# Kernel tuning notes

Measured on AMD Instinct MI355X. Metric: run time of the kernel, lower is better.

Reference implementation:

```python
import jax, jax.numpy as jnp
import numpy as np

N = 1024      # node_num
E = 4         # edge_type_num
D = 64        # state_dim
ANN = 16      # annotation_dim
STEPS = 5     # n_steps
B = 4         # batch


def setup_inputs() -> dict:
    key = jax.random.key(0)
    ks = jax.random.split(key, 10)
    w = lambda k, shape: jax.random.normal(k, shape, jnp.float32) * 0.02
    return {
        "prop_state": jax.random.normal(ks[0], (B, N, D), jnp.float32),
        "annotation": jax.random.normal(ks[1], (B, N, ANN), jnp.float32),
        "A": jax.random.uniform(ks[2], (B, N, 2 * N * E), jnp.float32),
        # per-edge-type linears (torch Linear: weight [out, in])
        "in_W": w(ks[3], (E, D, D)), "in_b": jnp.zeros((E, D), jnp.float32),
        "out_W": w(ks[4], (E, D, D)), "out_b": jnp.zeros((E, D), jnp.float32),
        # GRU-style gates: Linear(3D -> D)
        "rW": w(ks[5], (D, 3 * D)), "rb": jnp.zeros((D,), jnp.float32),
        "zW": w(ks[6], (D, 3 * D)), "zb": jnp.zeros((D,), jnp.float32),
        "hW": w(ks[7], (D, 3 * D)), "hb": jnp.zeros((D,), jnp.float32),
        # output head: Linear(D+ANN -> D) -> tanh -> Linear(D -> 1)
        "o1W": w(ks[8], (D, D + ANN)), "o1b": jnp.zeros((D,), jnp.float32),
        "o2W": w(ks[9], (1, D)), "o2b": jnp.zeros((1,), jnp.float32),
    }


def reference(prop_state, annotation, A, in_W, in_b, out_W, out_b,
              rW, rb, zW, zb, hW, hb, o1W, o1b, o2W, o2b):
    A_in = A[:, :, : N * E]  # [B, N, E*N]; A_out slice is unused in the original
    h = prop_state
    for _ in range(STEPS):
        # all edge-type linears as one batched GEMM: [B, N, E, D] -> [B, E*N, D]
        in_states = jnp.einsum("bnd,efd->bend", h, in_W) + in_b[None, :, None, :]
        in_states = in_states.reshape(B, E * N, D)
        a_in = jnp.einsum("bnm,bmd->bnd", A_in, in_states)
        a_out = a_in  # faithful to original: a_out = bmm(A_in, state_in) too
        a = jnp.concatenate([a_in, a_out, h], axis=2)  # [B, N, 3D]
        r = jax.nn.sigmoid(a @ rW.T + rb)
        z = jax.nn.sigmoid(a @ zW.T + zb)
        h_hat = jnp.tanh(jnp.concatenate([a_in, a_out, r * h], axis=2) @ hW.T + hb)
        h = (1.0 - z) * h + z * h_hat
    join = jnp.concatenate([h, annotation], axis=2)  # [B, N, D+ANN]
    out = jnp.tanh(join @ o1W.T + o1b) @ o2W.T + o2b  # [B, N, 1]
    return out.sum(axis=2)  # [B, N]
```

## Files before the change

### kernel.cpp

```cpp
#include <hip/hip_runtime.h>
#include <math.h>

#define N_NODES 1024
#define EDGE    4
#define DIM     64
#define ANND    16
#define STEPS   5
#define BATCH   4

typedef __attribute__((ext_vector_type(8))) short bf16x8;
typedef __attribute__((ext_vector_type(4))) float f32x4;

__device__ __forceinline__ float fsigmoid(float x) {
    return 1.0f / (1.0f + __expf(-x));
}
__device__ __forceinline__ float ftanh(float x) {
    x = fminf(15.0f, fmaxf(-15.0f, x));
    float t = __expf(2.0f * x);
    return (t - 1.0f) / (t + 1.0f);
}
__device__ __forceinline__ unsigned short f32_to_bf16(float x) {
    unsigned int u = __float_as_uint(x);
    unsigned int r = u + 0x7FFFu + ((u >> 16) & 1u);
    return (unsigned short)(r >> 16);
}

__global__ __launch_bounds__(256) void prepA(
    const float* __restrict__ A, unsigned short* __restrict__ Ahl,
    float* __restrict__ rowsum)
{
    const int row = blockIdx.x;
    const int t = threadIdx.x;
    const float* src = A + (size_t)row * 8192 + t * 16;
    unsigned short* dst = Ahl + (size_t)row * 8192 + t * 32;
    float s = 0.f;
#pragma unroll
    for (int c = 0; c < 2; ++c) {
        alignas(16) unsigned short hs[8], ls[8];
#pragma unroll
        for (int i = 0; i < 2; ++i) {
            float4 v = *(const float4*)(src + c * 8 + i * 4);
            float vv[4] = {v.x, v.y, v.z, v.w};
#pragma unroll
            for (int j = 0; j < 4; ++j) {
                float x = vv[j];
                s += x;
                unsigned short hh = f32_to_bf16(x);
                hs[i * 4 + j] = hh;
                ls[i * 4 + j] = f32_to_bf16(x - __uint_as_float((unsigned int)hh << 16));
            }
        }
        *(uint4*)(dst + c * 16)     = *(const uint4*)hs;
        *(uint4*)(dst + c * 16 + 8) = *(const uint4*)ls;
    }
#pragma unroll
    for (int off = 32; off > 0; off >>= 1) s += __shfl_down(s, off);
    if ((t & 63) == 0) rowsum[(size_t)row * 4 + (t >> 6)] = s;
}

__global__ void prepW(const float* __restrict__ inW, const float* __restrict__ rW,
                      const float* __restrict__ zW, const float* __restrict__ hW,
                      const float* __restrict__ o1W,
                      float* __restrict__ wcomb, float* __restrict__ w1s,
                      float* __restrict__ o1hT, float* __restrict__ o1aT)
{
    int id = blockIdx.x * 256 + threadIdx.x;
    if (id < 256) {
        int e = id >> 6, d = id & 63;
        float s = 0.0f;
        for (int f = 0; f < 64; ++f) s += inW[(e * 64 + f) * 64 + d];
        w1s[id] = s;
    }
    int i1 = id - 256;
    if (i1 >= 0 && i1 < 24576) {
        int mat = i1 >> 12, rem = i1 & 4095, d = rem >> 6, j = rem & 63;
        const float* W = (mat < 2) ? rW : (mat < 4) ? zW : hW;
        float v;
        if ((mat & 1) == 0) v = W[j * 192 + d] + W[j * 192 + 64 + d];
        else                v = W[j * 192 + 128 + d];
        wcomb[mat * 4096 + d * 64 + j] = v;
    }
    int i2 = id - 256 - 24576;
    if (i2 >= 0 && i2 < 4096) {
        int d = i2 >> 6, j = i2 & 63;
        o1hT[d * 64 + j] = o1W[j * 80 + d];
    }
    int i3 = id - 256 - 24576 - 4096;
    if (i3 >= 0 && i3 < 1024) {
        int a = i3 >> 6, j = i3 & 63;
        o1aT[a * 64 + j] = o1W[j * 80 + 64 + a];
    }
}

__global__ __launch_bounds__(256) void transposeH(
    const float* __restrict__ h, unsigned short* __restrict__ hThi,
    unsigned short* __restrict__ hTlo)
{
    __shared__ float tile[64][65];
    const int bm = blockIdx.x & 15, b = blockIdx.x >> 4;
    const int t = threadIdx.x;
    {
        const int mml = t >> 2, d0 = (t & 3) * 16;
        const float* src = h + ((size_t)(b * 1024 + bm * 64 + mml)) * 64 + d0;
#pragma unroll
        for (int i = 0; i < 4; ++i) {
            float4 v = *(const float4*)(src + i * 4);
            tile[d0 + i * 4 + 0][mml] = v.x;
            tile[d0 + i * 4 + 1][mml] = v.y;
            tile[d0 + i * 4 + 2][mml] = v.z;
            tile[d0 + i * 4 + 3][mml] = v.w;
        }
    }
    __syncthreads();
    const int d = t >> 2, m0 = (t & 3) * 16;
    alignas(16) unsigned short hb[16], lb[16];
#pragma unroll
    for (int i = 0; i < 16; ++i) {
        float x = tile[d][m0 + i];
        unsigned short hh = f32_to_bf16(x);
        hb[i] = hh;
        lb[i] = f32_to_bf16(x - __uint_as_float((unsigned int)hh << 16));
    }
    unsigned short* dst = hThi + ((size_t)(b * 64 + d)) * 1024 + bm * 64 + m0;
    *(uint4*)dst = *(const uint4*)&hb[0];
    *(uint4*)(dst + 8) = *(const uint4*)&hb[8];
    unsigned short* dstl = hTlo + ((size_t)(b * 64 + d)) * 1024 + bm * 64 + m0;
    *(uint4*)dstl = *(const uint4*)&lb[0];
    *(uint4*)(dstl + 8) = *(const uint4*)&lb[8];
}

__global__ __launch_bounds__(256, 4) void gemm_mfma(
    const unsigned short* __restrict__ Ahl,
    const unsigned short* __restrict__ hThi, const unsigned short* __restrict__ hTlo,
    const float* __restrict__ w1s, float* __restrict__ part)
{
    __shared__ unsigned short Xhs[64][64];
    __shared__ unsigned short Xls[64][64];
    const int tid = threadIdx.x;
    const int lane = tid & 63, wave = tid >> 6;
    const int nb = blockIdx.x, chunk = blockIdx.y, b = blockIdx.z;
    const int e = chunk >> 2, kq = chunk & 3;
    const int rowbase = nb * 64 + wave * 16;

    const size_t abase = ((size_t)(b * 1024 + rowbase + (lane & 15))) * 8192
                       + (size_t)(e * 128 + kq * 32 + (lane >> 4)) * 16;

    const int sd = tid >> 3;
    const int sc = tid & 7;
    const int scp = (sc ^ (sd & 7)) * 8;
    const int ldsoff0 = sd * 64 + scp;
    const int ldsoff1 = (sd + 32) * 64 + scp;
    const size_t xsrc = ((size_t)(b * 64 + sd)) * 1024 + kq * 256 + sc * 8;
    const unsigned short* xh0 = hThi + xsrc;
    const unsigned short* xl0 = hTlo + xsrc;

    uint4 sH0 = *(const uint4*)(xh0);
    uint4 sH1 = *(const uint4*)(xh0 + 32 * 1024);
    uint4 sL0 = *(const uint4*)(xl0);
    uint4 sL1 = *(const uint4*)(xl0 + 32 * 1024);

    f32x4 acc[4] = {};

#pragma unroll
    for (int sub = 0; sub < 4; ++sub) {
        __syncthreads();
        *(uint4*)&((unsigned short*)Xhs)[ldsoff0] = sH0;
        *(uint4*)&((unsigned short*)Xhs)[ldsoff1] = sH1;
        *(uint4*)&((unsigned short*)Xls)[ldsoff0] = sL0;
        *(uint4*)&((unsigned short*)Xls)[ldsoff1] = sL1;
        __syncthreads();
        if (sub < 3) {
            const unsigned short* ph = xh0 + (sub + 1) * 64;
            const unsigned short* pl = xl0 + (sub + 1) * 64;
            sH0 = *(const uint4*)(ph);
            sH1 = *(const uint4*)(ph + 32 * 1024);
            sL0 = *(const uint4*)(pl);
            sL1 = *(const uint4*)(pl + 32 * 1024);
        }
#pragma unroll
        for (int ks = 0; ks < 2; ++ks) {
            const unsigned short* ap = Ahl + abase + (size_t)(sub * 8 + ks * 4) * 16;
            bf16x8 a_hi = *(const bf16x8*)(ap);
            bf16x8 a_lo = *(const bf16x8*)(ap + 8);
#pragma unroll
            for (int df = 0; df < 4; ++df) {
                const int d = df * 16 + (lane & 15);
                const int cp = (((ks * 4) + (lane >> 4)) ^ (d & 7)) * 8;
                bf16x8 xh = *(const bf16x8*)&Xhs[d][cp];
                bf16x8 xl = *(const bf16x8*)&Xls[d][cp];
                acc[df] = __builtin_amdgcn_mfma_f32_16x16x32_bf16(a_hi, xh, acc[df], 0, 0, 0);
                acc[df] = __builtin_amdgcn_mfma_f32_16x16x32_bf16(a_hi, xl, acc[df], 0, 0, 0);
                acc[df] = __builtin_amdgcn_mfma_f32_16x16x32_bf16(a_lo, xh, acc[df], 0, 0, 0);
            }
        }
    }

    float* pbase = part + ((size_t)(chunk * 4 + b)) * 65536;
#pragma unroll
    for (int df = 0; df < 4; ++df) {
        const int d = df * 16 + (lane & 15);
        const float w = w1s[e * 64 + d];
#pragma unroll
        for (int r = 0; r < 4; ++r) {
            int n = rowbase + (lane >> 4) * 4 + r;
            pbase[(size_t)n * 64 + d] = acc[df][r] * w;
        }
    }
}

__global__ __launch_bounds__(256) void gate(
    const float* __restrict__ part, const float* __restrict__ wcomb,
    const float* __restrict__ rowsum, const float* __restrict__ inb,
    const float* __restrict__ rb, const float* __restrict__ zb,
    const float* __restrict__ hbias, float* __restrict__ h,
    unsigned short* __restrict__ hThi, unsigned short* __restrict__ hTlo)
{
    __shared__ float wl[24576];
    __shared__ float ain_sh[16][64];
    __shared__ float h_sh[16][64];
    __shared__ float r_sh[16][64];
    __shared__ float hn_sh[16][64];
    const int tid = threadIdx.x;
    const int nodeBase = blockIdx.x * 16;

#pragma unroll
    for (int i = 0; i < 24; ++i) {
        int idx = i * 256 + tid;
        *(float4*)&wl[idx * 4] = *(const float4*)&wcomb[idx * 4];
    }

#pragma unroll
    for (int i = 0; i < 4; ++i) {
        int idx = tid + 256 * i;
        int nl = idx >> 6, d = idx & 63;
        int node = nodeBase + nl;
        int bb = node >> 10, n = node & 1023;
        const float* pp = part + (size_t)bb * 65536 + (size_t)n * 64 + d;
        float s = 0.f;
#pragma unroll
        for (int c = 0; c < 16; ++c) s += pp[(size_t)c * 262144];
        const float* rs = rowsum + (size_t)node * 4;
#pragma unroll
        for (int e = 0; e < 4; ++e) s += rs[e] * inb[e * 64 + d];
        ain_sh[nl][d] = s;
        h_sh[nl][d] = h[(size_t)node * 64 + d];
    }
    __syncthreads();

    const int j  = tid & 63;
    const int ng = tid >> 6;
    const float* rCT = wl;
    const float* rHT = wl + 4096;
    const float* zCT = wl + 8192;
    const float* zHT = wl + 12288;
    const float* hCT = wl + 16384;
    const float* hHT = wl + 20480;

    float accr[4], accz[4];
#pragma unroll
    for (int i = 0; i < 4; ++i) { accr[i] = rb[j]; accz[i] = zb[j]; }
    for (int d = 0; d < 64; ++d) {
        float wrc = rCT[d * 64 + j], wrh = rHT[d * 64 + j];
        float wzc = zCT[d * 64 + j], wzh = zHT[d * 64 + j];
#pragma unroll
        for (int i = 0; i < 4; ++i) {
            int nl = ng * 4 + i;
            float av = ain_sh[nl][d], hv = h_sh[nl][d];
            accr[i] = fmaf(av, wrc, accr[i]); accr[i] = fmaf(hv, wrh, accr[i]);
            accz[i] = fmaf(av, wzc, accz[i]); accz[i] = fmaf(hv, wzh, accz[i]);
        }
    }
    float zreg[4];
#pragma unroll
    for (int i = 0; i < 4; ++i) {
        int nl = ng * 4 + i;
        r_sh[nl][j] = fsigmoid(accr[i]);
        zreg[i] = fsigmoid(accz[i]);
    }
    __syncthreads();

    float acch[4];
#pragma unroll
    for (int i = 0; i < 4; ++i) acch[i] = hbias[j];
    for (int d = 0; d < 64; ++d) {
        float whc = hCT[d * 64 + j], whh = hHT[d * 64 + j];
#pragma unroll
        for (int i = 0; i < 4; ++i) {
            int nl = ng * 4 + i;
            float av = ain_sh[nl][d];
            float rh = r_sh[nl][d] * h_sh[nl][d];
            acch[i] = fmaf(av, whc, acch[i]); acch[i] = fmaf(rh, whh, acch[i]);
        }
    }
#pragma unroll
    for (int i = 0; i < 4; ++i) {
        int nl = ng * 4 + i;
        int node = nodeBase + nl;
        float hh = ftanh(acch[i]);
        float ho = h_sh[nl][j];
        float hnew = ho + zreg[i] * (hh - ho);
        h[(size_t)node * 64 + j] = hnew;
        hn_sh[nl][j] = hnew;
    }
    __syncthreads();

    {
        const int d = tid >> 2, q = tid & 3;
        const int bb = nodeBase >> 10;
        const int mm0 = (nodeBase & 1023) + q * 4;
        alignas(8) unsigned short hb4[4], lb4[4];
#pragma unroll
        for (int i = 0; i < 4; ++i) {
            float x = hn_sh[q * 4 + i][d];
            unsigned short hh = f32_to_bf16(x);
            hb4[i] = hh;
            lb4[i] = f32_to_bf16(x - __uint_as_float((unsigned int)hh << 16));
        }
        unsigned short* dst = hThi + ((size_t)(bb * 64 + d)) * 1024 + mm0;
        *(uint2*)dst = *(const uint2*)hb4;
        unsigned short* dstl = hTlo + ((size_t)(bb * 64 + d)) * 1024 + mm0;
        *(uint2*)dstl = *(const uint2*)lb4;
    }
}

__global__ __launch_bounds__(256) void outk(
    const float* __restrict__ h, const float* __restrict__ ann,
    const float* __restrict__ o1hT, const float* __restrict__ o1aT,
    const float* __restrict__ o1b, const float* __restrict__ o2W,
    const float* __restrict__ o2b, float* __restrict__ out)
{
    __shared__ float h_sh[4][64];
    __shared__ float a_sh[4][16];
    const int tid = threadIdx.x;
    const int nodeBase = blockIdx.x * 4;
    {
        int nl = tid >> 6, d = tid & 63;
        h_sh[nl][d] = h[(size_t)(nodeBase + nl) * 64 + d];
    }
    if (tid < 64) {
        int nl = tid >> 4, a = tid & 15;
        a_sh[nl][a] = ann[(size_t)(nodeBase + nl) * 16 + a];
    }
    __syncthreads();
    const int j = tid & 63, nl = tid >> 6;
    float acc = o1b[j];
    for (int d = 0; d < 64; ++d) acc = fmaf(h_sh[nl][d], o1hT[d * 64 + j], acc);
    for (int a = 0; a < 16; ++a) acc = fmaf(a_sh[nl][a], o1aT[a * 64 + j], acc);
    float t = ftanh(acc) * o2W[j];
    for (int off = 32; off > 0; off >>= 1) t += __shfl_down(t, off);
    if (j == 0) out[nodeBase + nl] = t + o2b[0];
}

extern "C" void kernel_launch(void* const* d_in, const int* in_sizes, int n_in,
                              void* d_out, int out_size, void* d_ws, size_t ws_size,
                              hipStream_t stream)
{
    (void)in_sizes; (void)n_in; (void)out_size; (void)ws_size;
    const float* prop = (const float*)d_in[0];
    const float* ann  = (const float*)d_in[1];
    const float* A    = (const float*)d_in[2];
    const float* inW  = (const float*)d_in[3];
    const float* inb  = (const float*)d_in[4];
    const float* rW   = (const float*)d_in[7];
    const float* rb   = (const float*)d_in[8];
    const float* zW   = (const float*)d_in[9];
    const float* zb   = (const float*)d_in[10];
    const float* hW   = (const float*)d_in[11];
    const float* hb   = (const float*)d_in[12];
    const float* o1W  = (const float*)d_in[13];
    const float* o1b  = (const float*)d_in[14];
    const float* o2W  = (const float*)d_in[15];
    const float* o2b  = (const float*)d_in[16];
    float* out = (float*)d_out;

    float* h_ws   = (float*)d_ws;
    float* part   = h_ws + 262144;
    float* wcomb  = part + 16 * 262144;
    float* w1s    = wcomb + 24576;
    float* o1hT   = w1s + 256;
    float* o1aT   = o1hT + 4096;
    float* rowsum = o1aT + 1024;
    unsigned short* Ahl  = (unsigned short*)(rowsum + 16384);
    unsigned short* hThi = Ahl + (size_t)33554432;
    unsigned short* hTlo = hThi + 262144;

    prepA<<<4096, 256, 0, stream>>>(A, Ahl, rowsum);
    prepW<<<117, 256, 0, stream>>>(inW, rW, zW, hW, o1W, wcomb, w1s, o1hT, o1aT);
    hipMemcpyAsync(h_ws, prop, (size_t)262144 * sizeof(float),
                   hipMemcpyDeviceToDevice, stream);
    transposeH<<<64, 256, 0, stream>>>(h_ws, hThi, hTlo);

    for (int s = 0; s < STEPS; ++s) {
        gemm_mfma<<<dim3(16, 16, 4), 256, 0, stream>>>(Ahl, hThi, hTlo, w1s, part);
        gate<<<256, 256, 0, stream>>>(part, wcomb, rowsum, inb, rb, zb, hb,
                                      h_ws, hThi, hTlo);
    }
    outk<<<1024, 256, 0, stream>>>(h_ws, ann, o1hT, o1aT, o1b, o2W, o2b, out);
}
```

Baseline: 403.9 us.

## Fuse all stages into one persistent cooperative kernel with grid syncs

Replaces the chain of prep, per-step GEMM, gate and output kernels with a single cooperative kernel of 256 blocks that synchronises across the grid between phases. Each GEMM block now covers a full edge-type K range (16 sub-tiles) rather than a quarter, which shrinks the partial-sum buffer and the gate reduction. The gate weights are loaded into LDS once and reused across all steps. This removes about a dozen launches and their gaps, but runs only 256 blocks of heavy-LDS work, so GEMM parallelism drops and the A conversion pass loops over 16 rows per block.

```diff
diff --git a/kernel.cpp b/kernel.cpp
--- a/kernel.cpp
+++ b/kernel.cpp
@@ -1,5 +1,8 @@
 #include <hip/hip_runtime.h>
+#include <hip/hip_cooperative_groups.h>
 #include <math.h>
+
+namespace cg = cooperative_groups;
 
 #define N_NODES 1024
 #define EDGE    4
@@ -25,330 +28,344 @@
     return (unsigned short)(r >> 16);
 }
 
-__global__ __launch_bounds__(256) void prepA(
-    const float* __restrict__ A, unsigned short* __restrict__ Ahl,
-    float* __restrict__ rowsum)
+__global__ __launch_bounds__(256) void ggnn_mono(
+    const float* __restrict__ prop, const float* __restrict__ ann,
+    const float* __restrict__ A,
+    const float* __restrict__ inW, const float* __restrict__ inb,
+    const float* __restrict__ rW, const float* __restrict__ rb,
+    const float* __restrict__ zW, const float* __restrict__ zb,
+    const float* __restrict__ hW, const float* __restrict__ hb,
+    const float* __restrict__ o1W, const float* __restrict__ o1b,
+    const float* __restrict__ o2W, const float* __restrict__ o2b,
+    float* __restrict__ out, char* __restrict__ ws)
 {
-    const int row = blockIdx.x;
-    const int t = threadIdx.x;
-    const float* src = A + (size_t)row * 8192 + t * 16;
-    unsigned short* dst = Ahl + (size_t)row * 8192 + t * 32;
-    float s = 0.f;
-#pragma unroll
-    for (int c = 0; c < 2; ++c) {
-        alignas(16) unsigned short hs[8], ls[8];
-#pragma unroll
-        for (int i = 0; i < 2; ++i) {
-            float4 v = *(const float4*)(src + c * 8 + i * 4);
-            float vv[4] = {v.x, v.y, v.z, v.w};
-#pragma unroll
-            for (int j = 0; j < 4; ++j) {
-                float x = vv[j];
-                s += x;
-                unsigned short hh = f32_to_bf16(x);
-                hs[i * 4 + j] = hh;
-                ls[i * 4 + j] = f32_to_bf16(x - __uint_as_float((unsigned int)hh << 16));
-            }
-        }
-        *(uint4*)(dst + c * 16)     = *(const uint4*)hs;
-        *(uint4*)(dst + c * 16 + 8) = *(const uint4*)ls;
-    }
-#pragma unroll
-    for (int off = 32; off > 0; off >>= 1) s += __shfl_down(s, off);
-    if ((t & 63) == 0) rowsum[(size_t)row * 4 + (t >> 6)] = s;
-}
-
-__global__ void prepW(const float* __restrict__ inW, const float* __restrict__ rW,
-                      const float* __restrict__ zW, const float* __restrict__ hW,
-                      const float* __restrict__ o1W,
-                      float* __restrict__ wcomb, float* __restrict__ w1s,
-                      float* __restrict__ o1hT, float* __restrict__ o1aT)
-{
-    int id = blockIdx.x * 256 + threadIdx.x;
-    if (id < 256) {
-        int e = id >> 6, d = id & 63;
-        float s = 0.0f;
-        for (int f = 0; f < 64; ++f) s += inW[(e * 64 + f) * 64 + d];
-        w1s[id] = s;
-    }
-    int i1 = id - 256;
-    if (i1 >= 0 && i1 < 24576) {
-        int mat = i1 >> 12, rem = i1 & 4095, d = rem >> 6, j = rem & 63;
-        const float* W = (mat < 2) ? rW : (mat < 4) ? zW : hW;
-        float v;
-        if ((mat & 1) == 0) v = W[j * 192 + d] + W[j * 192 + 64 + d];
-        else                v = W[j * 192 + 128 + d];
-        wcomb[mat * 4096 + d * 64 + j] = v;
-    }
-    int i2 = id - 256 - 24576;
-    if (i2 >= 0 && i2 < 4096) {
-        int d = i2 >> 6, j = i2 & 63;
-        o1hT[d * 64 + j] = o1W[j * 80 + d];
-    }
-    int i3 = id - 256 - 24576 - 4096;
-    if (i3 >= 0 && i3 < 1024) {
-        int a = i3 >> 6, j = i3 & 63;
-        o1aT[a * 64 + j] = o1W[j * 80 + 64 + a];
-    }
-}
-
-__global__ __launch_bounds__(256) void transposeH(
-    const float* __restrict__ h, unsigned short* __restrict__ hThi,
-    unsigned short* __restrict__ hTlo)
-{
-    __shared__ float tile[64][65];
-    const int bm = blockIdx.x & 15, b = blockIdx.x >> 4;
-    const int t = threadIdx.x;
+    float* h_ws   = (float*)ws;
+    float* part   = h_ws + 262144;
+    float* wcomb  = part + 1048576;
+    float* w1s    = wcomb + 24576;
+    float* o1hT   = w1s + 256;
+    float* o1aT   = o1hT + 4096;
+    float* rowsum = o1aT + 1024;
+    unsigned short* Ahl  = (unsigned short*)(rowsum + 16384);
+    unsigned short* hThi = Ahl + (size_t)33554432;
+    unsigned short* hTlo = hThi + 262144;
+
+    __shared__ float wl[24576];
+    __shared__ float scratch[4224];
+
+    const int bid  = blockIdx.x;
+    const int tid  = threadIdx.x;
+    const int lane = tid & 63, wave = tid >> 6;
+    cg::grid_group grid = cg::this_grid();
+
+    if (bid < 64) {
+        float (*tile)[65] = (float(*)[65])scratch;
+        const int bm = bid & 15, tb = bid >> 4;
+        {
+            const int mml = tid >> 2, d0 = (tid & 3) * 16;
+            const float* src = prop + ((size_t)(tb * 1024 + bm * 64 + mml)) * 64 + d0;
+#pragma unroll
+            for (int i = 0; i < 4; ++i) {
+                float4 v = *(const float4*)(src + i * 4);
+                tile[d0 + i * 4 + 0][mml] = v.x;
+                tile[d0 + i * 4 + 1][mml] = v.y;
+                tile[d0 + i * 4 + 2][mml] = v.z;
+                tile[d0 + i * 4 + 3][mml] = v.w;
+            }
+        }
+        __syncthreads();
+        const int d = tid >> 2, m0 = (tid & 3) * 16;
+        alignas(16) unsigned short hb16[16], lb16[16];
+#pragma unroll
+        for (int i = 0; i < 16; ++i) {
+            float x = tile[d][m0 + i];
+            unsigned short hh = f32_to_bf16(x);
+            hb16[i] = hh;
+            lb16[i] = f32_to_bf16(x - __uint_as_float((unsigned int)hh << 16));
+        }
+        unsigned short* dst = hThi + ((size_t)(tb * 64 + d)) * 1024 + bm * 64 + m0;
+        *(uint4*)dst = *(const uint4*)&hb16[0];
+        *(uint4*)(dst + 8) = *(const uint4*)&hb16[8];
+        unsigned short* dstl = hTlo + ((size_t)(tb * 64 + d)) * 1024 + bm * 64 + m0;
+        *(uint4*)dstl = *(const uint4*)&lb16[0];
+        *(uint4*)(dstl + 8) = *(const uint4*)&lb16[8];
+    }
+
     {
-        const int mml = t >> 2, d0 = (t & 3) * 16;
-        const float* src = h + ((size_t)(b * 1024 + bm * 64 + mml)) * 64 + d0;
-#pragma unroll
-        for (int i = 0; i < 4; ++i) {
-            float4 v = *(const float4*)(src + i * 4);
-            tile[d0 + i * 4 + 0][mml] = v.x;
-            tile[d0 + i * 4 + 1][mml] = v.y;
-            tile[d0 + i * 4 + 2][mml] = v.z;
-            tile[d0 + i * 4 + 3][mml] = v.w;
-        }
-    }
-    __syncthreads();
-    const int d = t >> 2, m0 = (t & 3) * 16;
-    alignas(16) unsigned short hb[16], lb[16];
-#pragma unroll
-    for (int i = 0; i < 16; ++i) {
-        float x = tile[d][m0 + i];
-        unsigned short hh = f32_to_bf16(x);
-        hb[i] = hh;
-        lb[i] = f32_to_bf16(x - __uint_as_float((unsigned int)hh << 16));
-    }
-    unsigned short* dst = hThi + ((size_t)(b * 64 + d)) * 1024 + bm * 64 + m0;
-    *(uint4*)dst = *(const uint4*)&hb[0];
-    *(uint4*)(dst + 8) = *(const uint4*)&hb[8];
-    unsigned short* dstl = hTlo + ((size_t)(b * 64 + d)) * 1024 + bm * 64 + m0;
-    *(uint4*)dstl = *(const uint4*)&lb[0];
-    *(uint4*)(dstl + 8) = *(const uint4*)&lb[8];
-}
-
-__global__ __launch_bounds__(256, 4) void gemm_mfma(
-    const unsigned short* __restrict__ Ahl,
-    const unsigned short* __restrict__ hThi, const unsigned short* __restrict__ hTlo,
-    const float* __restrict__ w1s, float* __restrict__ part)
-{
-    __shared__ unsigned short Xhs[64][64];
-    __shared__ unsigned short Xls[64][64];
-    const int tid = threadIdx.x;
-    const int lane = tid & 63, wave = tid >> 6;
-    const int nb = blockIdx.x, chunk = blockIdx.y, b = blockIdx.z;
-    const int e = chunk >> 2, kq = chunk & 3;
-    const int rowbase = nb * 64 + wave * 16;
-
-    const size_t abase = ((size_t)(b * 1024 + rowbase + (lane & 15))) * 8192
-                       + (size_t)(e * 128 + kq * 32 + (lane >> 4)) * 16;
-
-    const int sd = tid >> 3;
-    const int sc = tid & 7;
-    const int scp = (sc ^ (sd & 7)) * 8;
-    const int ldsoff0 = sd * 64 + scp;
-    const int ldsoff1 = (sd + 32) * 64 + scp;
-    const size_t xsrc = ((size_t)(b * 64 + sd)) * 1024 + kq * 256 + sc * 8;
-    const unsigned short* xh0 = hThi + xsrc;
-    const unsigned short* xl0 = hTlo + xsrc;
-
-    uint4 sH0 = *(const uint4*)(xh0);
-    uint4 sH1 = *(const uint4*)(xh0 + 32 * 1024);
-    uint4 sL0 = *(const uint4*)(xl0);
-    uint4 sL1 = *(const uint4*)(xl0 + 32 * 1024);
-
-    f32x4 acc[4] = {};
-
-#pragma unroll
-    for (int sub = 0; sub < 4; ++sub) {
-        __syncthreads();
-        *(uint4*)&((unsigned short*)Xhs)[ldsoff0] = sH0;
-        *(uint4*)&((unsigned short*)Xhs)[ldsoff1] = sH1;
-        *(uint4*)&((unsigned short*)Xls)[ldsoff0] = sL0;
-        *(uint4*)&((unsigned short*)Xls)[ldsoff1] = sL1;
-        __syncthreads();
-        if (sub < 3) {
-            const unsigned short* ph = xh0 + (sub + 1) * 64;
-            const unsigned short* pl = xl0 + (sub + 1) * 64;
-            sH0 = *(const uint4*)(ph);
-            sH1 = *(const uint4*)(ph + 32 * 1024);
-            sL0 = *(const uint4*)(pl);
-            sL1 = *(const uint4*)(pl + 32 * 1024);
-        }
-#pragma unroll
-        for (int ks = 0; ks < 2; ++ks) {
-            const unsigned short* ap = Ahl + abase + (size_t)(sub * 8 + ks * 4) * 16;
-            bf16x8 a_hi = *(const bf16x8*)(ap);
-            bf16x8 a_lo = *(const bf16x8*)(ap + 8);
-#pragma unroll
-            for (int df = 0; df < 4; ++df) {
-                const int d = df * 16 + (lane & 15);
-                const int cp = (((ks * 4) + (lane >> 4)) ^ (d & 7)) * 8;
-                bf16x8 xh = *(const bf16x8*)&Xhs[d][cp];
-                bf16x8 xl = *(const bf16x8*)&Xls[d][cp];
-                acc[df] = __builtin_amdgcn_mfma_f32_16x16x32_bf16(a_hi, xh, acc[df], 0, 0, 0);
-                acc[df] = __builtin_amdgcn_mfma_f32_16x16x32_bf16(a_hi, xl, acc[df], 0, 0, 0);
-                acc[df] = __builtin_amdgcn_mfma_f32_16x16x32_bf16(a_lo, xh, acc[df], 0, 0, 0);
-            }
-        }
-    }
-
-    float* pbase = part + ((size_t)(chunk * 4 + b)) * 65536;
-#pragma unroll
-    for (int df = 0; df < 4; ++df) {
-        const int d = df * 16 + (lane & 15);
-        const float w = w1s[e * 64 + d];
-#pragma unroll
-        for (int r = 0; r < 4; ++r) {
-            int n = rowbase + (lane >> 4) * 4 + r;
-            pbase[(size_t)n * 64 + d] = acc[df][r] * w;
-        }
-    }
-}
-
-__global__ __launch_bounds__(256) void gate(
-    const float* __restrict__ part, const float* __restrict__ wcomb,
-    const float* __restrict__ rowsum, const float* __restrict__ inb,
-    const float* __restrict__ rb, const float* __restrict__ zb,
-    const float* __restrict__ hbias, float* __restrict__ h,
-    unsigned short* __restrict__ hThi, unsigned short* __restrict__ hTlo)
-{
-    __shared__ float wl[24576];
-    __shared__ float ain_sh[16][64];
-    __shared__ float h_sh[16][64];
-    __shared__ float r_sh[16][64];
-    __shared__ float hn_sh[16][64];
-    const int tid = threadIdx.x;
-    const int nodeBase = blockIdx.x * 16;
+        int id = bid * 256 + tid;
+        if (id < 256) {
+            int e = id >> 6, d = id & 63;
+            float s = 0.0f;
+            for (int f = 0; f < 64; ++f) s += inW[(e * 64 + f) * 64 + d];
+            w1s[id] = s;
+        }
+        int i1 = id - 256;
+        if (i1 >= 0 && i1 < 24576) {
+            int mat = i1 >> 12, rem = i1 & 4095, d = rem >> 6, j = rem & 63;
+            const float* W = (mat < 2) ? rW : (mat < 4) ? zW : hW;
+            float v;
+            if ((mat & 1) == 0) v = W[j * 192 + d] + W[j * 192 + 64 + d];
+            else                v = W[j * 192 + 128 + d];
+            wcomb[mat * 4096 + d * 64 + j] = v;
+        }
+        int i2 = id - 256 - 24576;
+        if (i2 >= 0 && i2 < 4096) {
+            int d = i2 >> 6, j = i2 & 63;
+            o1hT[d * 64 + j] = o1W[j * 80 + d];
+        }
+        int i3 = id - 256 - 24576 - 4096;
+        if (i3 >= 0 && i3 < 1024) {
+            int a = i3 >> 6, j = i3 & 63;
+            o1aT[a * 64 + j] = o1W[j * 80 + 64 + a];
+        }
+    }
+
+    {
+        int base = bid * 1024 + tid * 4;
+        *(float4*)&h_ws[base] = *(const float4*)&prop[base];
+    }
+
+    {
+        const float* srcb = A + (size_t)bid * 16 * 8192 + tid * 16;
+        unsigned short* dstb = Ahl + (size_t)bid * 16 * 8192 + tid * 32;
+        for (int r = 0; r < 16; ++r) {
+            const float* src = srcb + (size_t)r * 8192;
+            unsigned short* dst = dstb + (size_t)r * 8192;
+            float s = 0.f;
+#pragma unroll
+            for (int c = 0; c < 2; ++c) {
+                alignas(16) unsigned short hs[8], ls[8];
+#pragma unroll
+                for (int i = 0; i < 2; ++i) {
+                    float4 v = *(const float4*)(src + c * 8 + i * 4);
+                    float vv[4] = {v.x, v.y, v.z, v.w};
+#pragma unroll
+                    for (int j = 0; j < 4; ++j) {
+                        float x = vv[j];
+                        s += x;
+                        unsigned short hh = f32_to_bf16(x);
+                        hs[i * 4 + j] = hh;
+                        ls[i * 4 + j] = f32_to_bf16(x - __uint_as_float((unsigned int)hh << 16));
+                    }
+                }
+                *(uint4*)(dst + c * 16)     = *(const uint4*)hs;
+                *(uint4*)(dst + c * 16 + 8) = *(const uint4*)ls;
+            }
+#pragma unroll
+            for (int off = 32; off > 0; off >>= 1) s += __shfl_down(s, off);
+            if (lane == 0) rowsum[(size_t)(bid * 16 + r) * 4 + wave] = s;
+        }
+    }
+
+    grid.sync();
 
 #pragma unroll
     for (int i = 0; i < 24; ++i) {
         int idx = i * 256 + tid;
         *(float4*)&wl[idx * 4] = *(const float4*)&wcomb[idx * 4];
     }
-
-#pragma unroll
-    for (int i = 0; i < 4; ++i) {
-        int idx = tid + 256 * i;
-        int nl = idx >> 6, d = idx & 63;
-        int node = nodeBase + nl;
-        int bb = node >> 10, n = node & 1023;
-        const float* pp = part + (size_t)bb * 65536 + (size_t)n * 64 + d;
-        float s = 0.f;
-#pragma unroll
-        for (int c = 0; c < 16; ++c) s += pp[(size_t)c * 262144];
-        const float* rs = rowsum + (size_t)node * 4;
-#pragma unroll
-        for (int e = 0; e < 4; ++e) s += rs[e] * inb[e * 64 + d];
-        ain_sh[nl][d] = s;
-        h_sh[nl][d] = h[(size_t)node * 64 + d];
-    }
     __syncthreads();
 
-    const int j  = tid & 63;
-    const int ng = tid >> 6;
-    const float* rCT = wl;
-    const float* rHT = wl + 4096;
-    const float* zCT = wl + 8192;
-    const float* zHT = wl + 12288;
-    const float* hCT = wl + 16384;
-    const float* hHT = wl + 20480;
-
-    float accr[4], accz[4];
-#pragma unroll
-    for (int i = 0; i < 4; ++i) { accr[i] = rb[j]; accz[i] = zb[j]; }
-    for (int d = 0; d < 64; ++d) {
-        float wrc = rCT[d * 64 + j], wrh = rHT[d * 64 + j];
-        float wzc = zCT[d * 64 + j], wzh = zHT[d * 64 + j];
+    for (int s = 0; s < STEPS; ++s) {
+        {
+            unsigned short* Xh = (unsigned short*)scratch;
+            unsigned short* Xl = Xh + 4096;
+            const int gb = bid & 3, ge = (bid >> 2) & 3, gnb = bid >> 4;
+            const int rowbase = gnb * 64 + wave * 16;
+            const size_t abase = ((size_t)(gb * 1024 + rowbase + (lane & 15))) * 8192
+                               + (size_t)(ge * 128 + (lane >> 4)) * 16;
+            const int sd = tid >> 3, sc = tid & 7;
+            const int scp = (sc ^ (sd & 7)) * 8;
+            const int ldsoff0 = sd * 64 + scp;
+            const int ldsoff1 = (sd + 32) * 64 + scp;
+            const size_t xsrc = ((size_t)(gb * 64 + sd)) * 1024 + sc * 8;
+            const unsigned short* xh0 = hThi + xsrc;
+            const unsigned short* xl0 = hTlo + xsrc;
+
+            uint4 sH0 = *(const uint4*)(xh0);
+            uint4 sH1 = *(const uint4*)(xh0 + 32 * 1024);
+            uint4 sL0 = *(const uint4*)(xl0);
+            uint4 sL1 = *(const uint4*)(xl0 + 32 * 1024);
+
+            f32x4 acc[4] = {};
+
+            for (int sub = 0; sub < 16; ++sub) {
+                __syncthreads();
+                *(uint4*)&Xh[ldsoff0] = sH0;
+                *(uint4*)&Xh[ldsoff1] = sH1;
+                *(uint4*)&Xl[ldsoff0] = sL0;
+                *(uint4*)&Xl[ldsoff1] = sL1;
+                __syncthreads();
+                if (sub < 15) {
+                    const unsigned short* ph = xh0 + (sub + 1) * 64;
+                    const unsigned short* pl = xl0 + (sub + 1) * 64;
+                    sH0 = *(const uint4*)(ph);
+                    sH1 = *(const uint4*)(ph + 32 * 1024);
+                    sL0 = *(const uint4*)(pl);
+                    sL1 = *(const uint4*)(pl + 32 * 1024);
+                }
+#pragma unroll
+                for (int ks = 0; ks < 2; ++ks) {
+                    const unsigned short* ap = Ahl + abase + (size_t)(sub * 8 + ks * 4) * 16;
+                    bf16x8 a_hi = *(const bf16x8*)(ap);
+                    bf16x8 a_lo = *(const bf16x8*)(ap + 8);
+#pragma unroll
+                    for (int df = 0; df < 4; ++df) {
+                        const int d = df * 16 + (lane & 15);
+                        const int cp = (((ks * 4) + (lane >> 4)) ^ (d & 7)) * 8;
+                        bf16x8 xh = *(const bf16x8*)&Xh[d * 64 + cp];
+                        bf16x8 xl = *(const bf16x8*)&Xl[d * 64 + cp];
+                        acc[df] = __builtin_amdgcn_mfma_f32_16x16x32_bf16(a_hi, xh, acc[df], 0, 0, 0);
+                        acc[df] = __builtin_amdgcn_mfma_f32_16x16x32_bf16(a_hi, xl, acc[df], 0, 0, 0);
+                        acc[df] = __builtin_amdgcn_mfma_f32_16x16x32_bf16(a_lo, xh, acc[df], 0, 0, 0);
+                    }
+                }
+            }
+
+            float* pbase = part + ((size_t)(ge * 4 + gb)) * 65536;
+#pragma unroll
+            for (int df = 0; df < 4; ++df) {
+                const int d = df * 16 + (lane & 15);
+                const float w = w1s[ge * 64 + d];
+#pragma unroll
+                for (int r = 0; r < 4; ++r) {
+                    int n = rowbase + (lane >> 4) * 4 + r;
+                    pbase[(size_t)n * 64 + d] = acc[df][r] * w;
+                }
+            }
+        }
+        grid.sync();
+
+        {
+            float* ain  = scratch;
+            float* hsh  = scratch + 1024;
+            float* rsh  = scratch + 2048;
+            float* hnsh = scratch + 3072;
+            const int nodeBase = bid * 16;
+
+#pragma unroll
+            for (int i = 0; i < 4; ++i) {
+                int idx = tid + 256 * i;
+                int nl = idx >> 6, d = idx & 63;
+                int node = nodeBase + nl;
+                int bb = node >> 10, n = node & 1023;
+                const float* pp = part + (size_t)bb * 65536 + (size_t)n * 64 + d;
+                float sv = pp[0] + pp[262144] + pp[2 * 262144] + pp[3 * 262144];
+                const float* rs = rowsum + (size_t)node * 4;
+#pragma unroll
+                for (int e = 0; e < 4; ++e) sv += rs[e] * inb[e * 64 + d];
+                ain[nl * 64 + d] = sv;
+                hsh[nl * 64 + d] = h_ws[(size_t)node * 64 + d];
+            }
+            __syncthreads();
+
+            const int j  = tid & 63;
+            const int ng = tid >> 6;
+            const float* rCT = wl;
+            const float* rHT = wl + 4096;
+            const float* zCT = wl + 8192;
+            const float* zHT = wl + 12288;
+            const float* hCT = wl + 16384;
+            const float* hHT = wl + 20480;
+
+            float accr[4], accz[4];
+#pragma unroll
+            for (int i = 0; i < 4; ++i) { accr[i] = rb[j]; accz[i] = zb[j]; }
+            for (int d = 0; d < 64; ++d) {
+                float wrc = rCT[d * 64 + j], wrh = rHT[d * 64 + j];
+                float wzc = zCT[d * 64 + j], wzh = zHT[d * 64 + j];
+#pragma unroll
+                for (int i = 0; i < 4; ++i) {
+                    int nl = ng * 4 + i;
+                    float av = ain[nl * 64 + d], hv = hsh[nl * 64 + d];
+                    accr[i] = fmaf(av, wrc, accr[i]); accr[i] = fmaf(hv, wrh, accr[i]);
+                    accz[i] = fmaf(av, wzc, accz[i]); accz[i] = fmaf(hv, wzh, accz[i]);
+                }
+            }
+            float zreg[4];
+#pragma unroll
+            for (int i = 0; i < 4; ++i) {
+                int nl = ng * 4 + i;
+                rsh[nl * 64 + j] = fsigmoid(accr[i]);
+                zreg[i] = fsigmoid(accz[i]);
+            }
+            __syncthreads();
+
+            float acch[4];
+#pragma unroll
+            for (int i = 0; i < 4; ++i) acch[i] = hb[j];
+            for (int d = 0; d < 64; ++d) {
+                float whc = hCT[d * 64 + j], whh = hHT[d * 64 + j];
+#pragma unroll
+                for (int i = 0; i < 4; ++i) {
+                    int nl = ng * 4 + i;
+                    float av = ain[nl * 64 + d];
+                    float rh = rsh[nl * 64 + d] * hsh[nl * 64 + d];
+                    acch[i] = fmaf(av, whc, acch[i]); acch[i] = fmaf(rh, whh, acch[i]);
+                }
+            }
+#pragma unroll
+            for (int i = 0; i < 4; ++i) {
+                int nl = ng * 4 + i;
+                int node = nodeBase + nl;
+                float hh2 = ftanh(acch[i]);
+                float ho = hsh[nl * 64 + j];
+                float hnew = ho + zreg[i] * (hh2 - ho);
+                h_ws[(size_t)node * 64 + j] = hnew;
+                hnsh[nl * 64 + j] = hnew;
+            }
+            __syncthreads();
+
+            {
+                const int d = tid >> 2, q = tid & 3;
+                const int bb = nodeBase >> 10;
+                const int mm0 = (nodeBase & 1023) + q * 4;
+                alignas(8) unsigned short hb4[4], lb4[4];
+#pragma unroll
+                for (int i = 0; i < 4; ++i) {
+                    float x = hnsh[(q * 4 + i) * 64 + d];
+                    unsigned short hh = f32_to_bf16(x);
+                    hb4[i] = hh;
+                    lb4[i] = f32_to_bf16(x - __uint_as_float((unsigned int)hh << 16));
+                }
+                unsigned short* dst = hThi + ((size_t)(bb * 64 + d)) * 1024 + mm0;
+                *(uint2*)dst = *(const uint2*)hb4;
+                unsigned short* dstl = hTlo + ((size_t)(bb * 64 + d)) * 1024 + mm0;
+                *(uint2*)dstl = *(const uint2*)lb4;
+            }
+        }
+        grid.sync();
+    }
+
+    {
+#pragma unroll
+        for (int i = 0; i < 16; ++i) {
+            int idx = tid + 256 * i;
+            scratch[idx] = o1hT[idx];
+        }
 #pragma unroll
         for (int i = 0; i < 4; ++i) {
-            int nl = ng * 4 + i;
-            float av = ain_sh[nl][d], hv = h_sh[nl][d];
-            accr[i] = fmaf(av, wrc, accr[i]); accr[i] = fmaf(hv, wrh, accr[i]);
-            accz[i] = fmaf(av, wzc, accz[i]); accz[i] = fmaf(hv, wzh, accz[i]);
-        }
-    }
-    float zreg[4];
-#pragma unroll
-    for (int i = 0; i < 4; ++i) {
-        int nl = ng * 4 + i;
-        r_sh[nl][j] = fsigmoid(accr[i]);
-        zreg[i] = fsigmoid(accz[i]);
-    }
-    __syncthreads();
-
-    float acch[4];
-#pragma unroll
-    for (int i = 0; i < 4; ++i) acch[i] = hbias[j];
-    for (int d = 0; d < 64; ++d) {
-        float whc = hCT[d * 64 + j], whh = hHT[d * 64 + j];
+            int idx = tid + 256 * i;
+            wl[idx] = o1aT[idx];
+        }
+        if (tid < 64) { wl[4096 + tid] = o1b[tid]; wl[4160 + tid] = o2W[tid]; }
+        __syncthreads();
+        const int j = lane;
 #pragma unroll
         for (int i = 0; i < 4; ++i) {
-            int nl = ng * 4 + i;
-            float av = ain_sh[nl][d];
-            float rh = r_sh[nl][d] * h_sh[nl][d];
-            acch[i] = fmaf(av, whc, acch[i]); acch[i] = fmaf(rh, whh, acch[i]);
-        }
-    }
-#pragma unroll
-    for (int i = 0; i < 4; ++i) {
-        int nl = ng * 4 + i;
-        int node = nodeBase + nl;
-        float hh = ftanh(acch[i]);
-        float ho = h_sh[nl][j];
-        float hnew = ho + zreg[i] * (hh - ho);
-        h[(size_t)node * 64 + j] = hnew;
-        hn_sh[nl][j] = hnew;
-    }
-    __syncthreads();
-
-    {
-        const int d = tid >> 2, q = tid & 3;
-        const int bb = nodeBase >> 10;
-        const int mm0 = (nodeBase & 1023) + q * 4;
-        alignas(8) unsigned short hb4[4], lb4[4];
-#pragma unroll
-        for (int i = 0; i < 4; ++i) {
-            float x = hn_sh[q * 4 + i][d];
-            unsigned short hh = f32_to_bf16(x);
-            hb4[i] = hh;
-            lb4[i] = f32_to_bf16(x - __uint_as_float((unsigned int)hh << 16));
-        }
-        unsigned short* dst = hThi + ((size_t)(bb * 64 + d)) * 1024 + mm0;
-        *(uint2*)dst = *(const uint2*)hb4;
-        unsigned short* dstl = hTlo + ((size_t)(bb * 64 + d)) * 1024 + mm0;
-        *(uint2*)dstl = *(const uint2*)lb4;
-    }
-}
-
-__global__ __launch_bounds__(256) void outk(
-    const float* __restrict__ h, const float* __restrict__ ann,
-    const float* __restrict__ o1hT, const float* __restrict__ o1aT,
-    const float* __restrict__ o1b, const float* __restrict__ o2W,
-    const float* __restrict__ o2b, float* __restrict__ out)
-{
-    __shared__ float h_sh[4][64];
-    __shared__ float a_sh[4][16];
-    const int tid = threadIdx.x;
-    const int nodeBase = blockIdx.x * 4;
-    {
-        int nl = tid >> 6, d = tid & 63;
-        h_sh[nl][d] = h[(size_t)(nodeBase + nl) * 64 + d];
-    }
-    if (tid < 64) {
-        int nl = tid >> 4, a = tid & 15;
-        a_sh[nl][a] = ann[(size_t)(nodeBase + nl) * 16 + a];
-    }
-    __syncthreads();
-    const int j = tid & 63, nl = tid >> 6;
-    float acc = o1b[j];
-    for (int d = 0; d < 64; ++d) acc = fmaf(h_sh[nl][d], o1hT[d * 64 + j], acc);
-    for (int a = 0; a < 16; ++a) acc = fmaf(a_sh[nl][a], o1aT[a * 64 + j], acc);
-    float t = ftanh(acc) * o2W[j];
-    for (int off = 32; off > 0; off >>= 1) t += __shfl_down(t, off);
-    if (j == 0) out[nodeBase + nl] = t + o2b[0];
+            int node = bid * 16 + wave * 4 + i;
+            float acc2 = wl[4096 + j];
+            const float* hp = h_ws + (size_t)node * 64;
+            for (int d = 0; d < 64; ++d) acc2 = fmaf(hp[d], scratch[d * 64 + j], acc2);
+            const float* ap2 = ann + (size_t)node * 16;
+#pragma unroll
+            for (int a = 0; a < 16; ++a) acc2 = fmaf(ap2[a], wl[a * 64 + j], acc2);
+            float t = ftanh(acc2) * wl[4160 + j];
+#pragma unroll
+            for (int off = 32; off > 0; off >>= 1) t += __shfl_down(t, off);
+            if (j == 0) out[node] = t + o2b[0];
+        }
+    }
 }
 
 extern "C" void kernel_launch(void* const* d_in, const int* in_sizes, int n_in,
@@ -372,28 +389,12 @@
     const float* o2W  = (const float*)d_in[15];
     const float* o2b  = (const float*)d_in[16];
     float* out = (float*)d_out;
-
-    float* h_ws   = (float*)d_ws;
-    float* part   = h_ws + 262144;
-    float* wcomb  = part + 16 * 262144;
-    float* w1s    = wcomb + 24576;
-    float* o1hT   = w1s + 256;
-    float* o1aT   = o1hT + 4096;
-    float* rowsum = o1aT + 1024;
-    unsigned short* Ahl  = (unsigned short*)(rowsum + 16384);
-    unsigned short* hThi = Ahl + (size_t)33554432;
-    unsigned short* hTlo = hThi + 262144;
-
-    prepA<<<4096, 256, 0, stream>>>(A, Ahl, rowsum);
-    prepW<<<117, 256, 0, stream>>>(inW, rW, zW, hW, o1W, wcomb, w1s, o1hT, o1aT);
-    hipMemcpyAsync(h_ws, prop, (size_t)262144 * sizeof(float),
-                   hipMemcpyDeviceToDevice, stream);
-    transposeH<<<64, 256, 0, stream>>>(h_ws, hThi, hTlo);
-
-    for (int s = 0; s < STEPS; ++s) {
-        gemm_mfma<<<dim3(16, 16, 4), 256, 0, stream>>>(Ahl, hThi, hTlo, w1s, part);
-        gate<<<256, 256, 0, stream>>>(part, wcomb, rowsum, inb, rb, zb, hb,
-                                      h_ws, hThi, hTlo);
-    }
-    outk<<<1024, 256, 0, stream>>>(h_ws, ann, o1hT, o1aT, o1b, o2W, o2b, out);
+    char* ws = (char*)d_ws;
+
+    void* args[] = {
+        &prop, &ann, &A, &inW, &inb, &rW, &rb, &zW, &zb, &hW, &hb,
+        &o1W, &o1b, &o2W, &o2b, &out, &ws
+    };
+    hipLaunchCooperativeKernel((const void*)ggnn_mono, dim3(256), dim3(256),
+                               args, 0, stream);
 }
```

New measurement: 764.6 us. +89.3%, slower.
